# Performance work log

Hardware: AMD Instinct MI355X
Metric: run time of the kernel (lower is better)

The kernel has to match this reference:

```python
import jax, jax.numpy as jnp
import numpy as np

NUM_HEADS = 12
HEAD_DIM = 64


def setup_inputs() -> dict:
    key = jax.random.key(0)
    k1, k2, k3 = jax.random.split(key, 3)
    x = jax.random.normal(k1, (64, 768, 14, 14), dtype=jnp.float32)
    # 1x1 conv weights stored as [out_ch, in_ch]; scaled to keep softmax logits sane
    w_qkv = jax.random.normal(k2, (3 * NUM_HEADS * HEAD_DIM, 768), dtype=jnp.float32) * 0.02
    w_proj = jax.random.normal(k3, (768, NUM_HEADS * HEAD_DIM), dtype=jnp.float32) * 0.02
    return {"x": x, "w_qkv": w_qkv, "w_proj": w_proj}


def reference(x, w_qkv, w_proj):
    B, C, H, W = x.shape
    N = H * W
    scale = HEAD_DIM ** -0.25  # qk_scale=None -> head_dim**-0.25, applied to both q and k
    # 1x1 conv == channel matmul: [B,3*nh*dh,H,W]
    qkv = jnp.einsum('oc,bchw->bohw', w_qkv, x)
    # rearrange 'b (x y z) h w -> x b y (h w) z'
    qkv = qkv.reshape(B, 3, NUM_HEADS, HEAD_DIM, N).transpose(1, 0, 2, 4, 3)  # [3,B,nh,N,dh]
    q, k, v = qkv[0], qkv[1], qkv[2]
    attn = jnp.einsum('bhnd,bhmd->bhnm', q * scale, k * scale)  # [B,nh,N,N]
    attn = jax.nn.softmax(attn, axis=-1)
    out = jnp.einsum('bhnm,bhmd->bhnd', attn, v)  # [B,nh,N,dh]
    # rearrange 'b y (h w) z -> b (y z) h w'
    out = out.transpose(0, 1, 3, 2).reshape(B, NUM_HEADS * HEAD_DIM, H, W)
    out = jnp.einsum('oc,bchw->bohw', w_proj, out)  # proj 1x1 conv, no bias
    return out
```

## Files before the change

kernel.cpp:

```cpp
#include <hip/hip_runtime.h>
#include <cstdint>
#include <cstddef>

#define NH     12
#define DH     64
#define CIN    768
#define NPIX   196
#define NB     64
#define ROWS   (NB * NPIX)
#define QKV_OC 2304
#define NKT    12

typedef __attribute__((ext_vector_type(8))) _Float16 f16x8;
typedef __attribute__((ext_vector_type(4))) _Float16 f16x4;
typedef __attribute__((ext_vector_type(4))) float    f32x4;

#define MFMA16 __builtin_amdgcn_mfma_f32_16x16x32_f16

__global__ __launch_bounds__(256) void k_convert_w(const float* __restrict__ wq,
                                                   const float* __restrict__ wp,
                                                   _Float16* __restrict__ out) {
    int i = blockIdx.x * 256 + threadIdx.x;
    const int NQ = QKV_OC * CIN / 4;
    const int NT = NQ + (CIN * CIN) / 4;
    if (i >= NT) return;
    float4 v = (i < NQ) ? ((const float4*)wq)[i] : ((const float4*)wp)[i - NQ];
    f16x4 o = { (_Float16)v.x, (_Float16)v.y, (_Float16)v.z, (_Float16)v.w };
    ((f16x4*)out)[i] = o;
}

__global__ __launch_bounds__(256) void k_transpose_x(const float* __restrict__ x,
                                                     _Float16* __restrict__ Xt) {
    __shared__ __align__(16) _Float16 lds[NPIX][72];
    int t  = threadIdx.x;
    int b  = blockIdx.y, c0 = blockIdx.x * 64;
    const float* xp = x + ((size_t)b * CIN + c0) * NPIX;
    for (int idx = t; idx < 64 * 49; idx += 256) {
        int c = idx / 49, k = idx - c * 49;
        float4 v = *(const float4*)(xp + (size_t)c * NPIX + k * 4);
        int n = k * 4;
        lds[n][c]     = (_Float16)v.x;
        lds[n + 1][c] = (_Float16)v.y;
        lds[n + 2][c] = (_Float16)v.z;
        lds[n + 3][c] = (_Float16)v.w;
    }
    __syncthreads();
    int cs = t & 7, nn = t >> 3;
    for (int n = nn; n < NPIX; n += 32) {
        _Float16* dst = Xt + ((size_t)(b * NPIX + n)) * CIN + c0 + cs * 8;
        *(ulonglong2*)dst = *(const ulonglong2*)&lds[n][cs * 8];
    }
}

__device__ inline void gload16(const _Float16* g, _Float16* l) {
    __builtin_amdgcn_global_load_lds((const __attribute__((address_space(1))) void*)g,
                                     (__attribute__((address_space(3))) void*)l,
                                     16, 0, 0);
}

template<int NTN, bool PROJ>
__global__ __launch_bounds__(512, 2) void k_gemm2(const _Float16* __restrict__ A,
                                                  const _Float16* __restrict__ Bm,
                                                  _Float16* __restrict__ Cb,
                                                  float* __restrict__ Cf) {
    __shared__ __align__(16) _Float16 As[2][256 * 64];
    __shared__ __align__(16) _Float16 Bs[2][256 * 64];
    int tid = threadIdx.x;
    int w = tid >> 6, lane = tid & 63;

    int nwg = gridDim.x;
    int orig = blockIdx.x;
    int q = nwg >> 3, r = nwg & 7;
    int xcd = orig & 7, within = orig >> 3;
    int wg = (xcd < r ? xcd * (q + 1) : r * (q + 1) + (xcd - r) * q) + within;
    int bm = wg / NTN, bn = wg - bm * NTN;
    int m0 = bm * 256, n0 = bn * 256;

    int wr = w >> 2, wc = w & 3;
    int r16 = lane & 15, q4 = lane >> 4;

    int sr8  = (w << 3) + (lane >> 3);
    int swz8 = ((lane & 7) ^ (lane >> 3)) << 3;
    const _Float16* Ag = A  + (size_t)(m0 + sr8) * CIN + swz8;
    const _Float16* Bg = Bm + (size_t)(n0 + sr8) * CIN + swz8;

    auto stageA = [&](int buf, int kt) {
        const _Float16* g = Ag + kt * 64;
        _Float16* l0 = As[buf] + (w << 9);
        gload16(g,             l0);
        gload16(g +  64 * CIN, l0 + 4096);
        gload16(g + 128 * CIN, l0 + 8192);
        gload16(g + 192 * CIN, l0 + 12288);
    };
    auto stageB = [&](int buf, int kt) {
        const _Float16* g = Bg + kt * 64;
        _Float16* l0 = Bs[buf] + (w << 9);
        gload16(g,             l0);
        gload16(g +  64 * CIN, l0 + 4096);
        gload16(g + 128 * CIN, l0 + 8192);
        gload16(g + 192 * CIN, l0 + 12288);
    };

    int cS0 = ((q4)     ^ (r16 & 7)) << 3;
    int cS1 = ((q4 + 4) ^ (r16 & 7)) << 3;

    f32x4 acc[8][4];
#pragma unroll
    for (int i = 0; i < 8; i++)
#pragma unroll
        for (int j = 0; j < 4; j++) acc[i][j] = (f32x4){0.f, 0.f, 0.f, 0.f};

    stageA(0, 0); stageB(0, 0);
    stageA(1, 1); stageB(1, 1);
    asm volatile("s_waitcnt vmcnt(8)" ::: "memory");
    __builtin_amdgcn_sched_barrier(0);
    __builtin_amdgcn_s_barrier();

#pragma unroll 2
    for (int t = 0; t < NKT; ++t) {
        int bt = t & 1;
        const _Float16* Ab = As[bt] + ((wr << 7) + r16) * 64;
        const _Float16* Bb = Bs[bt] + ((wc << 6) + r16) * 64;
        bool pre = (t + 2 < NKT);

        f16x8 a0[4][2], a1[4][2], b0[2][2], b1[2][2];
#pragma unroll
        for (int i = 0; i < 4; i++) {
            a0[i][0] = *(const f16x8*)(Ab + (i << 10) + cS0);
            a0[i][1] = *(const f16x8*)(Ab + (i << 10) + cS1);
            a1[i][0] = *(const f16x8*)(Ab + 4096 + (i << 10) + cS0);
            a1[i][1] = *(const f16x8*)(Ab + 4096 + (i << 10) + cS1);
        }
#pragma unroll
        for (int j = 0; j < 2; j++) {
            b0[j][0] = *(const f16x8*)(Bb + (j << 10) + cS0);
            b0[j][1] = *(const f16x8*)(Bb + (j << 10) + cS1);
            b1[j][0] = *(const f16x8*)(Bb + 2048 + (j << 10) + cS0);
            b1[j][1] = *(const f16x8*)(Bb + 2048 + (j << 10) + cS1);
        }

        __builtin_amdgcn_s_setprio(1);
#pragma unroll
        for (int i = 0; i < 4; i++)
#pragma unroll
            for (int j = 0; j < 2; j++) {
                acc[i][j]     = MFMA16(a0[i][0], b0[j][0], acc[i][j],     0, 0, 0);
                acc[i][j]     = MFMA16(a0[i][1], b0[j][1], acc[i][j],     0, 0, 0);
                acc[4 + i][j] = MFMA16(a1[i][0], b0[j][0], acc[4 + i][j], 0, 0, 0);
                acc[4 + i][j] = MFMA16(a1[i][1], b0[j][1], acc[4 + i][j], 0, 0, 0);
            }
        __builtin_amdgcn_s_setprio(0);

        asm volatile("s_waitcnt lgkmcnt(0)" ::: "memory");
        __builtin_amdgcn_sched_barrier(0);
        __builtin_amdgcn_s_barrier();

        if (pre) { stageA(bt, t + 2); stageB(bt, t + 2); }

        __builtin_amdgcn_s_setprio(1);
#pragma unroll
        for (int i = 0; i < 4; i++)
#pragma unroll
            for (int j = 0; j < 2; j++) {
                acc[i][2 + j]     = MFMA16(a0[i][0], b1[j][0], acc[i][2 + j],     0, 0, 0);
                acc[i][2 + j]     = MFMA16(a0[i][1], b1[j][1], acc[i][2 + j],     0, 0, 0);
                acc[4 + i][2 + j] = MFMA16(a1[i][0], b1[j][0], acc[4 + i][2 + j], 0, 0, 0);
                acc[4 + i][2 + j] = MFMA16(a1[i][1], b1[j][1], acc[4 + i][2 + j], 0, 0, 0);
            }
        __builtin_amdgcn_s_setprio(0);

        if (pre) { asm volatile("s_waitcnt vmcnt(8)" ::: "memory"); }
        else     { asm volatile("s_waitcnt vmcnt(0)" ::: "memory"); }
        __builtin_amdgcn_sched_barrier(0);
        __builtin_amdgcn_s_barrier();
    }

    if (!PROJ) {
#pragma unroll
        for (int hh = 0; hh < 2; hh++)
#pragma unroll
            for (int i = 0; i < 4; i++)
#pragma unroll
                for (int rr = 0; rr < 4; rr++) {
                    int row = m0 + (wr << 7) + hh * 64 + i * 16 + q4 * 4 + rr;
                    _Float16* cp = Cb + (size_t)row * QKV_OC + n0 + (wc << 6) + r16;
#pragma unroll
                    for (int g = 0; g < 2; g++)
#pragma unroll
                        for (int j = 0; j < 2; j++)
                            cp[g * 32 + j * 16] = (_Float16)acc[hh * 4 + i][g * 2 + j][rr];
                }
    } else {
#pragma unroll
        for (int hh = 0; hh < 2; hh++)
#pragma unroll
            for (int i = 0; i < 4; i++) {
                int row = m0 + (wr << 7) + hh * 64 + i * 16 + q4 * 4;
                int b = row / NPIX;
                int n = row - b * NPIX;
#pragma unroll
                for (int g = 0; g < 2; g++)
#pragma unroll
                    for (int j = 0; j < 2; j++) {
                        int col = n0 + (wc << 6) + g * 32 + j * 16 + r16;
                        f32x4 a = acc[hh * 4 + i][g * 2 + j];
                        float4 o; o.x = a[0]; o.y = a[1]; o.z = a[2]; o.w = a[3];
                        *(float4*)(Cf + ((size_t)b * CIN + col) * NPIX + n) = o;
                    }
            }
    }
}

__global__ __launch_bounds__(256) void k_attn(const _Float16* __restrict__ qkv,
                                              _Float16* __restrict__ Ot) {
    __shared__ __align__(16) _Float16 Kl[208 * 64];
    __shared__ __align__(16) _Float16 Vt[64][216];
    __shared__ __align__(16) _Float16 Pl[4][16][216];
    int tid = threadIdx.x, wave = tid >> 6, lane = tid & 63;
    int bh = blockIdx.x;
    int b = bh / NH, h = bh - b * NH;
    const _Float16* base  = qkv + (size_t)b * NPIX * QKV_OC + h * DH;
    const _Float16* kb    = base + CIN;
    const _Float16* vbase = base + 2 * CIN;

    {
        int c8 = lane & 7;
#pragma unroll
        for (int rr = 0; rr < 7; ++rr) {
            int grp = wave + rr * 4;
            if (grp < 26) {
                int row = grp * 8 + (lane >> 3);
                const _Float16* src = kb + (size_t)row * QKV_OC + ((c8 ^ (row & 7)) << 3);
                gload16(src, Kl + row * 64 + (c8 << 3));
            }
        }
    }
    for (int task = tid; task < 208 * 8; task += 256) {
        int m = task >> 3, dc = (task & 7) * 8;
        f16x8 v = *(const f16x8*)(vbase + (size_t)m * QKV_OC + dc);
#pragma unroll
        for (int j = 0; j < 8; j++) Vt[dc + j][m] = v[j];
    }
    __syncthreads();

    int r16 = lane & 15, q4 = lane >> 4, r7 = r16 & 7;
    int kc0 = ((q4)     ^ r7) << 3;
    int kc1 = ((q4 + 4) ^ r7) << 3;
    const float s2 = 0.125f;

    for (int nt = wave; nt < 13; nt += 4) {
        f16x8 aq0 = *(const f16x8*)(base + (size_t)(nt * 16 + r16) * QKV_OC + q4 * 8);
        f16x8 aq1 = *(const f16x8*)(base + (size_t)(nt * 16 + r16) * QKV_OC + 32 + q4 * 8);
        f32x4 L[13];
#pragma unroll
        for (int mt = 0; mt < 13; ++mt) {
            const _Float16* kr = Kl + (mt * 16 + r16) * 64;
            f16x8 bk0 = *(const f16x8*)(kr + kc0);
            f16x8 bk1 = *(const f16x8*)(kr + kc1);
            f32x4 s = {0.f, 0.f, 0.f, 0.f};
            s = MFMA16(aq0, bk0, s, 0, 0, 0);
            s = MFMA16(aq1, bk1, s, 0, 0, 0);
            L[mt] = s;
        }
        float mx[4] = {-1e30f, -1e30f, -1e30f, -1e30f};
#pragma unroll
        for (int mt = 0; mt < 13; ++mt)
#pragma unroll
            for (int r = 0; r < 4; ++r) {
                float lv = L[mt][r] * s2;
                if (mt == 12 && r16 >= 4) lv = -1e30f;
                L[mt][r] = lv;
                mx[r] = fmaxf(mx[r], lv);
            }
#pragma unroll
        for (int r = 0; r < 4; ++r)
            for (int off = 1; off < 16; off <<= 1)
                mx[r] = fmaxf(mx[r], __shfl_xor(mx[r], off));
        float sm[4] = {0.f, 0.f, 0.f, 0.f};
#pragma unroll
        for (int mt = 0; mt < 13; ++mt)
#pragma unroll
            for (int r = 0; r < 4; ++r) {
                float p = exp2f((L[mt][r] - mx[r]) * 1.44269504f);
                sm[r] += p;
                Pl[wave][q4 * 4 + r][mt * 16 + r16] = (_Float16)p;
            }
#pragma unroll
        for (int r = 0; r < 4; ++r)
            for (int off = 1; off < 16; off <<= 1)
                sm[r] += __shfl_xor(sm[r], off);

        f32x4 oacc[4];
#pragma unroll
        for (int di = 0; di < 4; ++di) oacc[di] = (f32x4){0.f, 0.f, 0.f, 0.f};
#pragma unroll
        for (int mc = 0; mc < 6; ++mc) {
            f16x8 ap = *(const f16x8*)&Pl[wave][r16][mc * 32 + q4 * 8];
#pragma unroll
            for (int di = 0; di < 4; ++di) {
                f16x8 bv = *(const f16x8*)&Vt[di * 16 + r16][mc * 32 + q4 * 8];
                oacc[di] = MFMA16(ap, bv, oacc[di], 0, 0, 0);
            }
        }
        {
            _Float16 z = (_Float16)0.f;
            f16x8 zz = (f16x8){z, z, z, z, z, z, z, z};
            f16x8 ap = (q4 < 2) ? *(const f16x8*)&Pl[wave][r16][192 + q4 * 8] : zz;
#pragma unroll
            for (int di = 0; di < 4; ++di) {
                f16x8 bv = (q4 < 2) ? *(const f16x8*)&Vt[di * 16 + r16][192 + q4 * 8] : zz;
                oacc[di] = MFMA16(ap, bv, oacc[di], 0, 0, 0);
            }
        }
#pragma unroll
        for (int r = 0; r < 4; ++r) {
            int n = nt * 16 + q4 * 4 + r;
            if (n < NPIX) {
                float rinv = 1.0f / sm[r];
                _Float16* op = Ot + (size_t)(b * NPIX + n) * CIN + h * DH + r16;
#pragma unroll
                for (int di = 0; di < 4; ++di)
                    op[di * 16] = (_Float16)(oacc[di][r] * rinv);
            }
        }
    }
}

extern "C" void kernel_launch(void* const* d_in, const int* in_sizes, int n_in,
                              void* d_out, int out_size, void* d_ws, size_t ws_size,
                              hipStream_t stream) {
    const float* x  = (const float*)d_in[0];
    const float* wq = (const float*)d_in[1];
    const float* wp = (const float*)d_in[2];
    float* out = (float*)d_out;
    char* ws = (char*)d_ws;

    _Float16* Xt  = (_Float16*)(ws);
    _Float16* W   = (_Float16*)(ws + 20447232);
    _Float16* qkv = (_Float16*)(ws + 25165824);
    _Float16* Ot  = (_Float16*)(ws + 86507520);
    _Float16* Wq = W;
    _Float16* Wp = W + (size_t)QKV_OC * CIN;

    hipLaunchKernelGGL(k_convert_w, dim3(2304), dim3(256), 0, stream, wq, wp, W);
    hipLaunchKernelGGL(k_transpose_x, dim3(12, 64), dim3(256), 0, stream, x, Xt);
    hipLaunchKernelGGL((k_gemm2<9, false>), dim3(49 * 9), dim3(512), 0, stream,
                       Xt, Wq, qkv, (float*)nullptr);
    hipLaunchKernelGGL(k_attn, dim3(768), dim3(256), 0, stream, qkv, Ot);
    hipLaunchKernelGGL((k_gemm2<3, true>), dim3(49 * 3), dim3(512), 0, stream,
                       Ot, Wp, (_Float16*)nullptr, out);
}
```

Before: 140.0 us.

## Rework GEMM to 1024-thread blocks with 32-wide K tiles and 64x64 warp tiles

New measurement: 141.2 us. Within noise of the previous version (+0.8%).

```diff
diff --git a/kernel.cpp b/kernel.cpp
--- a/kernel.cpp
+++ b/kernel.cpp
@@ -9,7 +9,7 @@
 #define NB     64
 #define ROWS   (NB * NPIX)
 #define QKV_OC 2304
-#define NKT    12
+#define NKT2   24
 
 typedef __attribute__((ext_vector_type(8))) _Float16 f16x8;
 typedef __attribute__((ext_vector_type(4))) _Float16 f16x4;
@@ -59,12 +59,12 @@
 }
 
 template<int NTN, bool PROJ>
-__global__ __launch_bounds__(512, 2) void k_gemm2(const _Float16* __restrict__ A,
-                                                  const _Float16* __restrict__ Bm,
-                                                  _Float16* __restrict__ Cb,
-                                                  float* __restrict__ Cf) {
-    __shared__ __align__(16) _Float16 As[2][256 * 64];
-    __shared__ __align__(16) _Float16 Bs[2][256 * 64];
+__global__ __launch_bounds__(1024, 4) void k_gemm2(const _Float16* __restrict__ A,
+                                                   const _Float16* __restrict__ Bm,
+                                                   _Float16* __restrict__ Cb,
+                                                   float* __restrict__ Cf) {
+    __shared__ __align__(16) _Float16 As[2][256 * 32];
+    __shared__ __align__(16) _Float16 Bs[2][256 * 32];
     int tid = threadIdx.x;
     int w = tid >> 6, lane = tid & 63;
 
@@ -79,76 +79,47 @@
     int wr = w >> 2, wc = w & 3;
     int r16 = lane & 15, q4 = lane >> 4;
 
-    int sr8  = (w << 3) + (lane >> 3);
-    int swz8 = ((lane & 7) ^ (lane >> 3)) << 3;
-    const _Float16* Ag = A  + (size_t)(m0 + sr8) * CIN + swz8;
-    const _Float16* Bg = Bm + (size_t)(n0 + sr8) * CIN + swz8;
-
-    auto stageA = [&](int buf, int kt) {
-        const _Float16* g = Ag + kt * 64;
-        _Float16* l0 = As[buf] + (w << 9);
-        gload16(g,             l0);
-        gload16(g +  64 * CIN, l0 + 4096);
-        gload16(g + 128 * CIN, l0 + 8192);
-        gload16(g + 192 * CIN, l0 + 12288);
-    };
-    auto stageB = [&](int buf, int kt) {
-        const _Float16* g = Bg + kt * 64;
-        _Float16* l0 = Bs[buf] + (w << 9);
-        gload16(g,             l0);
-        gload16(g +  64 * CIN, l0 + 4096);
-        gload16(g + 128 * CIN, l0 + 8192);
-        gload16(g + 192 * CIN, l0 + 12288);
-    };
-
-    int cS0 = ((q4)     ^ (r16 & 7)) << 3;
-    int cS1 = ((q4 + 4) ^ (r16 & 7)) << 3;
-
-    f32x4 acc[8][4];
-#pragma unroll
-    for (int i = 0; i < 8; i++)
+    int srow = (w << 4) + (lane >> 2);
+    int gc8  = (((lane & 3) ^ ((lane >> 3) & 3)) << 3);
+    const _Float16* Ag = A  + (size_t)(m0 + srow) * CIN + gc8;
+    const _Float16* Bg = Bm + (size_t)(n0 + srow) * CIN + gc8;
+
+    auto stageA = [&](int buf, int kt) { gload16(Ag + kt * 32, As[buf] + (w << 9)); };
+    auto stageB = [&](int buf, int kt) { gload16(Bg + kt * 32, Bs[buf] + (w << 9)); };
+
+    int cS = ((q4 ^ ((r16 >> 1) & 3)) << 3);
+
+    f32x4 acc[4][4];
+#pragma unroll
+    for (int i = 0; i < 4; i++)
 #pragma unroll
         for (int j = 0; j < 4; j++) acc[i][j] = (f32x4){0.f, 0.f, 0.f, 0.f};
 
     stageA(0, 0); stageB(0, 0);
     stageA(1, 1); stageB(1, 1);
-    asm volatile("s_waitcnt vmcnt(8)" ::: "memory");
+    asm volatile("s_waitcnt vmcnt(2)" ::: "memory");
     __builtin_amdgcn_sched_barrier(0);
     __builtin_amdgcn_s_barrier();
 
 #pragma unroll 2
-    for (int t = 0; t < NKT; ++t) {
+    for (int t = 0; t < NKT2; ++t) {
         int bt = t & 1;
-        const _Float16* Ab = As[bt] + ((wr << 7) + r16) * 64;
-        const _Float16* Bb = Bs[bt] + ((wc << 6) + r16) * 64;
-        bool pre = (t + 2 < NKT);
-
-        f16x8 a0[4][2], a1[4][2], b0[2][2], b1[2][2];
-#pragma unroll
-        for (int i = 0; i < 4; i++) {
-            a0[i][0] = *(const f16x8*)(Ab + (i << 10) + cS0);
-            a0[i][1] = *(const f16x8*)(Ab + (i << 10) + cS1);
-            a1[i][0] = *(const f16x8*)(Ab + 4096 + (i << 10) + cS0);
-            a1[i][1] = *(const f16x8*)(Ab + 4096 + (i << 10) + cS1);
-        }
-#pragma unroll
-        for (int j = 0; j < 2; j++) {
-            b0[j][0] = *(const f16x8*)(Bb + (j << 10) + cS0);
-            b0[j][1] = *(const f16x8*)(Bb + (j << 10) + cS1);
-            b1[j][0] = *(const f16x8*)(Bb + 2048 + (j << 10) + cS0);
-            b1[j][1] = *(const f16x8*)(Bb + 2048 + (j << 10) + cS1);
-        }
+        const _Float16* Ab = As[bt] + (wr << 11) + r16 * 32 + cS;
+        const _Float16* Bb = Bs[bt] + (wc << 11) + r16 * 32 + cS;
+        bool pre = (t + 2 < NKT2);
+
+        f16x8 a[4], b[4];
+#pragma unroll
+        for (int i = 0; i < 4; i++) a[i] = *(const f16x8*)(Ab + (i << 9));
+#pragma unroll
+        for (int j = 0; j < 4; j++) b[j] = *(const f16x8*)(Bb + (j << 9));
 
         __builtin_amdgcn_s_setprio(1);
 #pragma unroll
         for (int i = 0; i < 4; i++)
 #pragma unroll
-            for (int j = 0; j < 2; j++) {
-                acc[i][j]     = MFMA16(a0[i][0], b0[j][0], acc[i][j],     0, 0, 0);
-                acc[i][j]     = MFMA16(a0[i][1], b0[j][1], acc[i][j],     0, 0, 0);
-                acc[4 + i][j] = MFMA16(a1[i][0], b0[j][0], acc[4 + i][j], 0, 0, 0);
-                acc[4 + i][j] = MFMA16(a1[i][1], b0[j][1], acc[4 + i][j], 0, 0, 0);
-            }
+            for (int j = 0; j < 2; j++)
+                acc[i][j] = MFMA16(a[i], b[j], acc[i][j], 0, 0, 0);
         __builtin_amdgcn_s_setprio(0);
 
         asm volatile("s_waitcnt lgkmcnt(0)" ::: "memory");
@@ -161,15 +132,11 @@
 #pragma unroll
         for (int i = 0; i < 4; i++)
 #pragma unroll
-            for (int j = 0; j < 2; j++) {
-                acc[i][2 + j]     = MFMA16(a0[i][0], b1[j][0], acc[i][2 + j],     0, 0, 0);
-                acc[i][2 + j]     = MFMA16(a0[i][1], b1[j][1], acc[i][2 + j],     0, 0, 0);
-                acc[4 + i][2 + j] = MFMA16(a1[i][0], b1[j][0], acc[4 + i][2 + j], 0, 0, 0);
-                acc[4 + i][2 + j] = MFMA16(a1[i][1], b1[j][1], acc[4 + i][2 + j], 0, 0, 0);
-            }
+            for (int j = 2; j < 4; j++)
+                acc[i][j] = MFMA16(a[i], b[j], acc[i][j], 0, 0, 0);
         __builtin_amdgcn_s_setprio(0);
 
-        if (pre) { asm volatile("s_waitcnt vmcnt(8)" ::: "memory"); }
+        if (pre) { asm volatile("s_waitcnt vmcnt(2)" ::: "memory"); }
         else     { asm volatile("s_waitcnt vmcnt(0)" ::: "memory"); }
         __builtin_amdgcn_sched_barrier(0);
         __builtin_amdgcn_s_barrier();
@@ -177,37 +144,29 @@
 
     if (!PROJ) {
 #pragma unroll
-        for (int hh = 0; hh < 2; hh++)
-#pragma unroll
-            for (int i = 0; i < 4; i++)
-#pragma unroll
-                for (int rr = 0; rr < 4; rr++) {
-                    int row = m0 + (wr << 7) + hh * 64 + i * 16 + q4 * 4 + rr;
-                    _Float16* cp = Cb + (size_t)row * QKV_OC + n0 + (wc << 6) + r16;
-#pragma unroll
-                    for (int g = 0; g < 2; g++)
-#pragma unroll
-                        for (int j = 0; j < 2; j++)
-                            cp[g * 32 + j * 16] = (_Float16)acc[hh * 4 + i][g * 2 + j][rr];
-                }
+        for (int rt = 0; rt < 4; rt++)
+#pragma unroll
+            for (int rr = 0; rr < 4; rr++) {
+                int row = m0 + (wr << 6) + rt * 16 + q4 * 4 + rr;
+                _Float16* cp = Cb + (size_t)row * QKV_OC + n0 + (wc << 6) + r16;
+#pragma unroll
+                for (int ct = 0; ct < 4; ct++)
+                    cp[ct * 16] = (_Float16)acc[rt][ct][rr];
+            }
     } else {
 #pragma unroll
-        for (int hh = 0; hh < 2; hh++)
-#pragma unroll
-            for (int i = 0; i < 4; i++) {
-                int row = m0 + (wr << 7) + hh * 64 + i * 16 + q4 * 4;
-                int b = row / NPIX;
-                int n = row - b * NPIX;
-#pragma unroll
-                for (int g = 0; g < 2; g++)
-#pragma unroll
-                    for (int j = 0; j < 2; j++) {
-                        int col = n0 + (wc << 6) + g * 32 + j * 16 + r16;
-                        f32x4 a = acc[hh * 4 + i][g * 2 + j];
-                        float4 o; o.x = a[0]; o.y = a[1]; o.z = a[2]; o.w = a[3];
-                        *(float4*)(Cf + ((size_t)b * CIN + col) * NPIX + n) = o;
-                    }
-            }
+        for (int rt = 0; rt < 4; rt++) {
+            int row = m0 + (wr << 6) + rt * 16 + q4 * 4;
+            int b = row / NPIX;
+            int n = row - b * NPIX;
+#pragma unroll
+            for (int ct = 0; ct < 4; ct++) {
+                int col = n0 + (wc << 6) + ct * 16 + r16;
+                f32x4 a = acc[rt][ct];
+                float4 o; o.x = a[0]; o.y = a[1]; o.z = a[2]; o.w = a[3];
+                *(float4*)(Cf + ((size_t)b * CIN + col) * NPIX + n) = o;
+            }
+        }
     }
 }
 
@@ -344,9 +303,9 @@
 
     hipLaunchKernelGGL(k_convert_w, dim3(2304), dim3(256), 0, stream, wq, wp, W);
     hipLaunchKernelGGL(k_transpose_x, dim3(12, 64), dim3(256), 0, stream, x, Xt);
-    hipLaunchKernelGGL((k_gemm2<9, false>), dim3(49 * 9), dim3(512), 0, stream,
+    hipLaunchKernelGGL((k_gemm2<9, false>), dim3(49 * 9), dim3(1024), 0, stream,
                        Xt, Wq, qkv, (float*)nullptr);
     hipLaunchKernelGGL(k_attn, dim3(768), dim3(256), 0, stream, qkv, Ot);
-    hipLaunchKernelGGL((k_gemm2<3, true>), dim3(49 * 3), dim3(512), 0, stream,
+    hipLaunchKernelGGL((k_gemm2<3, true>), dim3(49 * 3), dim3(1024), 0, stream,
                        Ot, Wp, (_Float16*)nullptr, out);
 }
```
